# Optimization experiments

Hardware: AMD Instinct MI355X
Metric: run time of the kernel (lower is better)

Reference implementation:

```python
import jax, jax.numpy as jnp
import numpy as np

B, C, T, D = 4, 64, 256, 256   # batch, channel, time, in_feat
H, DK, OUT = 4, 64, 256        # heads, d_k, out_feat
MIN_VALUE = float(np.finfo(np.float32).min)


def _complex_linear(xr, xi, wr, wi, br, bi):
    # ComplexLinear: (fc_r(xr) - fc_i(xi), fc_r(xi) + fc_i(xr))
    out_r = (xr @ wr + br) - (xi @ wi + bi)
    out_i = (xi @ wr + br) + (xr @ wi + bi)
    return out_r, out_i


def setup_inputs() -> dict:
    key = jax.random.key(0)
    ks = jax.random.split(key, 23)
    s = 1.0 / np.sqrt(D)
    inp = {}
    names = ['q_r', 'q_i', 'k_r', 'k_i', 'v_r', 'v_i']
    for i, n in enumerate(names):
        inp[n] = jax.random.normal(ks[i], (B, C, T, D), dtype=jnp.float32)
    inp['mask'] = jnp.ones((B, 1, C), dtype=jnp.int32)
    pi = 6
    for proj in ['q', 'k', 'v', 'o']:
        out_dim = OUT if proj == 'o' else D
        inp[f'w{proj}_r'] = jax.random.normal(ks[pi], (D, out_dim), dtype=jnp.float32) * s; pi += 1
        inp[f'w{proj}_i'] = jax.random.normal(ks[pi], (D, out_dim), dtype=jnp.float32) * s; pi += 1
        inp[f'b{proj}_r'] = jax.random.normal(ks[pi], (out_dim,), dtype=jnp.float32) * 0.01; pi += 1
        inp[f'b{proj}_i'] = jax.random.normal(ks[pi], (out_dim,), dtype=jnp.float32) * 0.01; pi += 1
    return inp


def _split_heads(x):
    # (B, C, T, D) -> (B, H, T, C, DK)  [view + transpose(1,3)]
    return x.reshape(B, C, T, H, DK).transpose(0, 3, 2, 1, 4)


def _attention(q_r, q_i, k_r, k_i, v_r, v_i, mask,
               wq_r, wq_i, bq_r, bq_i, wk_r, wk_i, bk_r, bk_i,
               wv_r, wv_i, bv_r, bv_i, wo_r, wo_i, bo_r, bo_i):
    qr, qi = _complex_linear(q_r, q_i, wq_r, wq_i, bq_r, bq_i)
    kr, ki = _complex_linear(k_r, k_i, wk_r, wk_i, bk_r, bk_i)
    vr, vi = _complex_linear(v_r, v_i, wv_r, wv_i, bv_r, bv_i)
    qr, qi, kr, ki, vr, vi = map(_split_heads, (qr, qi, kr, ki, vr, vi))

    # scores = conj(q) @ k^T  (conjugate_transpose_matmul_conjugate), scaled by 1/sqrt(d_k)
    scale = 1.0 / np.sqrt(DK)
    s_r = (jnp.einsum('bhtcd,bhted->bhtce', qr, kr)
           + jnp.einsum('bhtcd,bhted->bhtce', qi, ki)) * scale
    s_i = (jnp.einsum('bhtcd,bhted->bhtce', qr, ki)
           - jnp.einsum('bhtcd,bhted->bhtce', qi, kr)) * scale

    # amplitude softmax with masking (mask: (B,1,C) -> (B,1,1,1,C), eq(0))
    mask_b = (mask == 0)[:, None, None]  # (B,1,1,1,C)
    amp = jnp.sqrt(s_r * s_r + s_i * s_i)
    amp = jnp.where(mask_b, MIN_VALUE, amp)
    sc = jax.nn.softmax(amp, axis=-1) / amp
    a_r = jnp.where(mask_b, 0.0, sc * s_r)
    a_i = jnp.where(mask_b, 0.0, sc * s_i)

    # complex matmul attn @ v
    x_r = (jnp.einsum('bhtce,bhted->bhtcd', a_r, vr)
           - jnp.einsum('bhtce,bhted->bhtcd', a_i, vi))
    x_i = (jnp.einsum('bhtce,bhted->bhtcd', a_i, vr)
           + jnp.einsum('bhtce,bhted->bhtcd', a_r, vi))

    # (B,H,T,C,DK) -> (B,C,T,H*DK)
    x_r = x_r.transpose(0, 3, 2, 1, 4).reshape(B, C, T, H * DK)
    x_i = x_i.transpose(0, 3, 2, 1, 4).reshape(B, C, T, H * DK)
    return _complex_linear(x_r, x_i, wo_r, wo_i, bo_r, bo_i)


def reference(q_r, q_i, k_r, k_i, v_r, v_i, mask,
              wq_r, wq_i, bq_r, bq_i, wk_r, wk_i, bk_r, bk_i,
              wv_r, wv_i, bv_r, bv_i, wo_r, wo_i, bo_r, bo_i):
    return _attention(q_r, q_i, k_r, k_i, v_r, v_i, mask,
                      wq_r, wq_i, bq_r, bq_i, wk_r, wk_i, bk_r, bk_i,
                      wv_r, wv_i, bv_r, bv_i, wo_r, wo_i, bo_r, bo_i)
```

## Files before the change

### kernel.cpp

```cpp
#include <hip/hip_runtime.h>
#include <hip/hip_bf16.h>
#include <cstddef>

#define MIN_VALUE_F (-3.402823466e38f)


typedef __attribute__((ext_vector_type(8))) __bf16 bfrag;
typedef __attribute__((ext_vector_type(4))) float f32x4;

__device__ __forceinline__ float bf2f(unsigned int u) {
    union { unsigned int i; float f; } v; v.i = u << 16; return v.f;
}
__device__ __forceinline__ unsigned short f2bf(float f) {
    union { float f; unsigned int i; } v; v.f = f;
    return (unsigned short)((v.i + 0x7fffu + ((v.i >> 16) & 1u)) >> 16);
}
__device__ __forceinline__ unsigned int cvt2(float a, float b) {
    __hip_bfloat16 lo = __float2bfloat16(a);
    __hip_bfloat16 hi = __float2bfloat16(b);
    union { __hip_bfloat16 h[2]; unsigned int u; } x;
    x.h[0] = lo; x.h[1] = hi;
    return x.u;
}
__device__ __forceinline__ bfrag negf(bfrag v) {
    union { bfrag b; unsigned int u[4]; } x; x.b = v;
    #pragma unroll
    for (int i = 0; i < 4; ++i) x.u[i] ^= 0x80008000u;
    return x.b;
}

typedef __attribute__((address_space(3))) void lds_void_t;
typedef const __attribute__((address_space(1))) void gmem_void_t;
__device__ __forceinline__ void glds16(const void* g, void* l) {
    __builtin_amdgcn_global_load_lds((gmem_void_t*)g, (lds_void_t*)l, 16, 0, 0);
}

__device__ __forceinline__ bfrag rdfrag(const unsigned short* arr, int row, int slot) {
    const int s = slot ^ (row & 7);
    return *(const bfrag*)&arr[row * 64 + s * 8];
}

__global__ __launch_bounds__(256)
void wprep_kernel(const float* __restrict__ w0, const float* __restrict__ w1,
                  const float* __restrict__ w2, const float* __restrict__ w3,
                  const float* __restrict__ w4, const float* __restrict__ w5,
                  unsigned short* __restrict__ dst)
{
    const int my = blockIdx.y;
    const float* wsrc[6] = {w0, w1, w2, w3, w4, w5};
    const float* w = wsrc[my];
    const int cid = blockIdx.x * 256 + threadIdx.x;
    const int img = cid >> 10;
    const int nb = img >> 2, s = img & 3;
    const int u0 = (cid & 1023) << 3;
    const int n_loc = u0 >> 6;
    const int k_src = (u0 & 63) ^ ((n_loc & 7) << 3);
    const int n = nb * 128 + n_loc;
    const int kbase = s * 64 + k_src;
    unsigned int p[4];
    #pragma unroll
    for (int jj = 0; jj < 4; ++jj) {
        const float a = w[(size_t)(kbase + 2 * jj) * 256 + n];
        const float b = w[(size_t)(kbase + 2 * jj + 1) * 256 + n];
        p[jj] = cvt2(a, b);
    }
    uint4 q; q.x = p[0]; q.y = p[1]; q.z = p[2]; q.w = p[3];
    *(uint4*)&dst[(size_t)my * 65536 + img * 8192 + u0] = q;
}

__global__ __launch_bounds__(512, 2)
void proj_mfma(const float* __restrict__ xq_r, const float* __restrict__ xq_i,
               const float* __restrict__ xk_r, const float* __restrict__ xk_i,
               const float* __restrict__ xv_r, const float* __restrict__ xv_i,
               const unsigned short* __restrict__ wimg,
               const float* __restrict__ bq_r, const float* __restrict__ bq_i,
               const float* __restrict__ bk_r, const float* __restrict__ bk_i,
               const float* __restrict__ bv_r, const float* __restrict__ bv_i,
               unsigned short* __restrict__ ws_out)
{
    __shared__ __align__(16) unsigned short SH[32768];
    unsigned short* As_r = SH;
    unsigned short* As_i = SH + 8192;
    unsigned short* Ws_r = SH + 16384;
    unsigned short* Ws_i = SH + 24576;

    const int pz = blockIdx.z;
    const float *xr, *xi, *br_, *bi_;
    if (pz == 0)      { xr = xq_r; xi = xq_i; br_ = bq_r; bi_ = bq_i; }
    else if (pz == 1) { xr = xk_r; xi = xk_i; br_ = bk_r; bi_ = bk_i; }
    else              { xr = xv_r; xi = xv_i; br_ = bv_r; bi_ = bv_i; }
    const unsigned short* wr_img = wimg + (size_t)pz * 131072;
    const unsigned short* wi_img = wr_img + 65536;
    unsigned short* outr = ws_out + (size_t)pz * 2 * 16777216;
    unsigned short* outi = outr + 16777216;

    const int tid = threadIdx.x;
    const int lane = tid & 63, wv = tid >> 6;
    const int l15 = lane & 15;
    const int wm = (wv >> 2) * 64, wn = (wv & 3) * 32;
    const int m0 = blockIdx.x * 128;
    const int nb = blockIdx.y;

    const int srow = tid >> 2;
    const int skq = (tid & 3) << 4;
    const int swz = (srow & 7) << 3;
    const int rowb = srow * 64;
    const float* arp = xr + (size_t)(m0 + srow) * 256 + skq;
    const float* aip = xi + (size_t)(m0 + srow) * 256 + skq;
    const uint4* wr32 = (const uint4*)(wr_img + nb * 4 * 8192);
    const uint4* wi32 = (const uint4*)(wi_img + nb * 4 * 8192);

    f32x4 accR[4][2] = {}, accI[4][2] = {};
    float4 ar4[4], ai4[4];
    uint4 wbr0, wbr1, wbi0, wbi1;

    auto load_step = [&](int s) {
        const float* a = arp + s * 64;
        const float* b = aip + s * 64;
        #pragma unroll
        for (int j = 0; j < 4; ++j) {
            ar4[j] = ((const float4*)a)[j];
            ai4[j] = ((const float4*)b)[j];
        }
        wbr0 = wr32[s * 1024 + tid];
        wbr1 = wr32[s * 1024 + 512 + tid];
        wbi0 = wi32[s * 1024 + tid];
        wbi1 = wi32[s * 1024 + 512 + tid];
    };
    auto write_stage = [&]() {
        uint4 p0, p1, q0, q1;
        p0.x = cvt2(ar4[0].x, ar4[0].y); p0.y = cvt2(ar4[0].z, ar4[0].w);
        p0.z = cvt2(ar4[1].x, ar4[1].y); p0.w = cvt2(ar4[1].z, ar4[1].w);
        p1.x = cvt2(ar4[2].x, ar4[2].y); p1.y = cvt2(ar4[2].z, ar4[2].w);
        p1.z = cvt2(ar4[3].x, ar4[3].y); p1.w = cvt2(ar4[3].z, ar4[3].w);
        q0.x = cvt2(ai4[0].x, ai4[0].y); q0.y = cvt2(ai4[0].z, ai4[0].w);
        q0.z = cvt2(ai4[1].x, ai4[1].y); q0.w = cvt2(ai4[1].z, ai4[1].w);
        q1.x = cvt2(ai4[2].x, ai4[2].y); q1.y = cvt2(ai4[2].z, ai4[2].w);
        q1.z = cvt2(ai4[3].x, ai4[3].y); q1.w = cvt2(ai4[3].z, ai4[3].w);
        *(uint4*)&As_r[rowb + (skq ^ swz)] = p0;
        *(uint4*)&As_r[rowb + ((skq + 8) ^ swz)] = p1;
        *(uint4*)&As_i[rowb + (skq ^ swz)] = q0;
        *(uint4*)&As_i[rowb + ((skq + 8) ^ swz)] = q1;
        *(uint4*)&Ws_r[tid * 8] = wbr0;
        *(uint4*)&Ws_r[4096 + tid * 8] = wbr1;
        *(uint4*)&Ws_i[tid * 8] = wbi0;
        *(uint4*)&Ws_i[4096 + tid * 8] = wbi1;
    };

    load_step(0);
    write_stage();
    __syncthreads();

    #pragma unroll
    for (int s = 0; s < 4; ++s) {
        if (s < 3) load_step(s + 1);
        #pragma unroll
        for (int ks = 0; ks < 2; ++ks) {
            const int kb = ks * 32 + ((lane >> 4) << 3);
            bfrag ar[4], ai[4], nai[4];
            #pragma unroll
            for (int mf = 0; mf < 4; ++mf) {
                const int m = wm + mf * 16 + l15;
                const int idx = m * 64 + (kb ^ ((m & 7) << 3));
                ar[mf] = *(const bfrag*)&As_r[idx];
                ai[mf] = *(const bfrag*)&As_i[idx];
                nai[mf] = negf(ai[mf]);
            }
            #pragma unroll
            for (int nf = 0; nf < 2; ++nf) {
                const int n = wn + nf * 16 + l15;
                const int idx = n * 64 + (kb ^ ((n & 7) << 3));
                const bfrag brf = *(const bfrag*)&Ws_r[idx];
                const bfrag bif = *(const bfrag*)&Ws_i[idx];
                #pragma unroll
                for (int mf = 0; mf < 4; ++mf) {
                    accR[mf][nf] = __builtin_amdgcn_mfma_f32_16x16x32_bf16(ar[mf], brf, accR[mf][nf], 0, 0, 0);
                    accR[mf][nf] = __builtin_amdgcn_mfma_f32_16x16x32_bf16(nai[mf], bif, accR[mf][nf], 0, 0, 0);
                    accI[mf][nf] = __builtin_amdgcn_mfma_f32_16x16x32_bf16(ai[mf], brf, accI[mf][nf], 0, 0, 0);
                    accI[mf][nf] = __builtin_amdgcn_mfma_f32_16x16x32_bf16(ar[mf], bif, accI[mf][nf], 0, 0, 0);
                }
            }
        }
        __syncthreads();
        if (s < 3) { write_stage(); __syncthreads(); }
    }

    const int bc = m0 >> 8, b = bc >> 6, c = bc & 63, t0 = m0 & 255;
    const int rowL = (lane >> 4) << 2;
    #pragma unroll
    for (int nf = 0; nf < 2; ++nf) {
        const int n_loc = wn + nf * 16 + l15;
        const int n_glob = nb * 128 + n_loc;
        const int hs = n_loc >> 6, dk = n_loc & 63;
        const float vbr = br_[n_glob], vbi = bi_[n_glob];
        const float addR = vbr - vbi, addI = vbr + vbi;
        #pragma unroll
        for (int mf = 0; mf < 4; ++mf) {
            const int tr = wm + mf * 16 + rowL;
            #pragma unroll
            for (int r = 0; r < 4; ++r) {
                const int L = hs * 8192 + (tr + r) * 64 + dk;
                SH[L] = f2bf(accR[mf][nf][r] + addR);
                SH[16384 + L] = f2bf(accI[mf][nf][r] + addI);
            }
        }
    }
    __syncthreads();
    const int h0 = nb * 2;
    #pragma unroll
    for (int p = 0; p < 4; ++p) {
        const int L = p * 4096 + tid * 8;
        const int hs2 = L >> 13, tr2 = (L >> 6) & 127, dk2 = L & 63;
        const size_t g = (((size_t)(b * 4 + h0 + hs2) * 256 + (t0 + tr2)) * 64 + c) * 64 + dk2;
        *(uint4*)&outr[g] = *(const uint4*)&SH[L];
        *(uint4*)&outi[g] = *(const uint4*)&SH[16384 + L];
    }
}

__global__ __launch_bounds__(256)
void attn_mfma(const unsigned short* __restrict__ Qg_r, const unsigned short* __restrict__ Qg_i,
               const unsigned short* __restrict__ Kg_r, const unsigned short* __restrict__ Kg_i,
               const unsigned short* __restrict__ Vg_r, const unsigned short* __restrict__ Vg_i,
               const int* __restrict__ mask,
               unsigned short* __restrict__ Xr, unsigned short* __restrict__ Xi)
{
    __shared__ __align__(16) unsigned short sQr[4096], sQi[4096];
    __shared__ __align__(16) unsigned short sKr[4096], sKi[4096];
    __shared__ __align__(16) unsigned short sVr[4608], sVi[4608];
    __shared__ int smask[64];

    const int bht = blockIdx.x;
    const int b = bht >> 10;
    const int h = (bht >> 8) & 3;
    const int t = bht & 255;
    const size_t base = (size_t)bht * 4096;
    const int tid = threadIdx.x;
    const int lane = tid & 63, wv = tid >> 6;
    const int l15 = lane & 15, hi = lane >> 4;

    const int ep = (lane & 31) * 2;
    const int dch = wv * 2 + (lane >> 5);
    const unsigned short* vr0p = Vg_r + base + (size_t)ep * 64 + dch * 8;
    const unsigned short* vi0p = Vg_i + base + (size_t)ep * 64 + dch * 8;
    const uint4 vr0 = *(const uint4*)vr0p;
    const uint4 vr1 = *(const uint4*)(vr0p + 64);
    const uint4 vi0 = *(const uint4*)vi0p;
    const uint4 vi1 = *(const uint4*)(vi0p + 64);

    #pragma unroll
    for (int i = 0; i < 2; ++i) {
        const int ch = wv * 128 + i * 64 + lane;
        const int r = ch >> 3, cg = ch & 7;
        const int so = r * 64 + ((cg ^ (r & 7)) << 3);
        const int dofs = (wv * 128 + i * 64) << 3;
        glds16(Qg_r + base + so, &sQr[dofs]);
        glds16(Qg_i + base + so, &sQi[dofs]);
        glds16(Kg_r + base + so, &sKr[dofs]);
        glds16(Kg_i + base + so, &sKi[dofs]);
    }
    if (tid < 64) smask[tid] = mask[b * 64 + tid];

    {
        union { uint4 v; unsigned short s[8]; } ar0, ar1, ai0, ai1;
        ar0.v = vr0; ar1.v = vr1; ai0.v = vi0; ai1.v = vi1;
        #pragma unroll
        for (int j = 0; j < 8; ++j) {
            const int d = dch * 8 + j;
            *(unsigned int*)&sVr[d * 72 + ep] = (unsigned)ar0.s[j] | ((unsigned)ar1.s[j] << 16);
            *(unsigned int*)&sVi[d * 72 + ep] = (unsigned)ai0.s[j] | ((unsigned)ai1.s[j] << 16);
        }
    }
    __syncthreads();

    const int cq = wv * 16 + l15;
    f32x4 aR[4] = {}, aI[4] = {};
    #pragma unroll
    for (int ks = 0; ks < 2; ++ks) {
        const int slot = ks * 4 + hi;
        const bfrag qr = rdfrag(sQr, cq, slot);
        const bfrag qi = rdfrag(sQi, cq, slot);
        const bfrag nqi = negf(qi);
        #pragma unroll
        for (int et = 0; et < 4; ++et) {
            const int re = et * 16 + l15;
            const bfrag kr = rdfrag(sKr, re, slot);
            const bfrag ki = rdfrag(sKi, re, slot);
            aR[et] = __builtin_amdgcn_mfma_f32_16x16x32_bf16(kr, qr, aR[et], 0, 0, 0);
            aR[et] = __builtin_amdgcn_mfma_f32_16x16x32_bf16(ki, qi, aR[et], 0, 0, 0);
            aI[et] = __builtin_amdgcn_mfma_f32_16x16x32_bf16(ki, qr, aI[et], 0, 0, 0);
            aI[et] = __builtin_amdgcn_mfma_f32_16x16x32_bf16(kr, nqi, aI[et], 0, 0, 0);
        }
    }
    __syncthreads();

    const float scale = 0.125f;
    float amp[4][4], ex[4][4];
    float mx = MIN_VALUE_F;
    #pragma unroll
    for (int et = 0; et < 4; ++et) {
        #pragma unroll
        for (int r = 0; r < 4; ++r) {
            const float sr = aR[et][r] * scale;
            const float si = aI[et][r] * scale;
            float a = sqrtf(fmaf(sr, sr, si * si));
            if (smask[et * 16 + hi * 4 + r] == 0) a = MIN_VALUE_F;
            amp[et][r] = a;
            mx = fmaxf(mx, a);
        }
    }
    mx = fmaxf(mx, __shfl_xor(mx, 16, 64));
    mx = fmaxf(mx, __shfl_xor(mx, 32, 64));
    float sm = 0.f;
    #pragma unroll
    for (int et = 0; et < 4; ++et) {
        #pragma unroll
        for (int r = 0; r < 4; ++r) {
            const float e_ = expf(amp[et][r] - mx);
            ex[et][r] = e_; sm += e_;
        }
    }
    sm += __shfl_xor(sm, 16, 64);
    sm += __shfl_xor(sm, 32, 64);

    #pragma unroll
    for (int et = 0; et < 4; ++et) {
        float pr[4], pi[4];
        #pragma unroll
        for (int r = 0; r < 4; ++r) {
            const float w = ex[et][r] * __builtin_amdgcn_rcpf(sm * amp[et][r]);
            pr[r] = w * (aR[et][r] * scale);
            pi[r] = w * (aI[et][r] * scale);
        }
        const int pidx = cq * 64 + ((et * 16 + hi * 4) ^ ((cq & 7) << 3));
        uint2 ur, ui;
        ur.x = cvt2(pr[0], pr[1]); ur.y = cvt2(pr[2], pr[3]);
        ui.x = cvt2(pi[0], pi[1]); ui.y = cvt2(pi[2], pi[3]);
        *(uint2*)&sQr[pidx] = ur;
        *(uint2*)&sQi[pidx] = ui;
    }
    __syncthreads();

    f32x4 xR4[4] = {}, xI4[4] = {};
    #pragma unroll
    for (int ks = 0; ks < 2; ++ks) {
        const int slot = ks * 4 + hi;
        const bfrag pr = rdfrag(sQr, cq, slot);
        const bfrag pi = rdfrag(sQi, cq, slot);
        const bfrag npi = negf(pi);
        #pragma unroll
        for (int dt = 0; dt < 4; ++dt) {
            const int rd = dt * 16 + l15;
            const bfrag vr = *(const bfrag*)&sVr[rd * 72 + ks * 32 + hi * 8];
            const bfrag vi = *(const bfrag*)&sVi[rd * 72 + ks * 32 + hi * 8];
            xR4[dt] = __builtin_amdgcn_mfma_f32_16x16x32_bf16(pr, vr, xR4[dt], 0, 0, 0);
            xR4[dt] = __builtin_amdgcn_mfma_f32_16x16x32_bf16(npi, vi, xR4[dt], 0, 0, 0);
            xI4[dt] = __builtin_amdgcn_mfma_f32_16x16x32_bf16(pi, vr, xI4[dt], 0, 0, 0);
            xI4[dt] = __builtin_amdgcn_mfma_f32_16x16x32_bf16(pr, vi, xI4[dt], 0, 0, 0);
        }
    }

    #pragma unroll
    for (int dt = 0; dt < 4; ++dt) {
        #pragma unroll
        for (int r = 0; r < 4; ++r) {
            const int c = wv * 16 + hi * 4 + r;
            const size_t o = (((size_t)(b * 64 + c) * 256) + t) * 256 + h * 64 + dt * 16 + l15;
            Xr[o] = f2bf(xR4[dt][r]);
            Xi[o] = f2bf(xI4[dt][r]);
        }
    }
}

__global__ __launch_bounds__(512, 2)
void oproj_mfma(const unsigned short* __restrict__ Xr_g, const unsigned short* __restrict__ Xi_g,
                const unsigned short* __restrict__ wimg,
                const float* __restrict__ bo_r, const float* __restrict__ bo_i,
                float* __restrict__ outr, float* __restrict__ outi)
{
    __shared__ __align__(16) unsigned short SH[32768];
    unsigned short* As_r = SH;
    unsigned short* As_i = SH + 8192;
    unsigned short* Ws_r = SH + 16384;
    unsigned short* Ws_i = SH + 24576;

    const int tid = threadIdx.x;
    const int lane = tid & 63, wv = tid >> 6;
    const int l15 = lane & 15;
    const int wm = (wv >> 2) * 64, wn = (wv & 3) * 32;
    const int m0 = blockIdx.x * 128;
    const int nb = blockIdx.y;

    const int srow = tid >> 2;
    const int skq = (tid & 3) << 4;
    const int swz = (srow & 7) << 3;
    const int rowb = srow * 64;
    const unsigned short* xrp = Xr_g + (size_t)(m0 + srow) * 256 + skq;
    const unsigned short* xip = Xi_g + (size_t)(m0 + srow) * 256 + skq;
    const uint4* wr32 = (const uint4*)(wimg + nb * 4 * 8192);
    const uint4* wi32 = (const uint4*)(wimg + 65536 + nb * 4 * 8192);

    f32x4 accR[4][2] = {}, accI[4][2] = {};
    uint4 xbr0, xbr1, xbi0, xbi1, wbr0, wbr1, wbi0, wbi1;

    auto load_step = [&](int s) {
        const uint4* a = (const uint4*)(xrp + s * 64);
        const uint4* bpt = (const uint4*)(xip + s * 64);
        xbr0 = a[0]; xbr1 = a[1];
        xbi0 = bpt[0]; xbi1 = bpt[1];
        wbr0 = wr32[s * 1024 + tid];
        wbr1 = wr32[s * 1024 + 512 + tid];
        wbi0 = wi32[s * 1024 + tid];
        wbi1 = wi32[s * 1024 + 512 + tid];
    };
    auto write_stage = [&]() {
        *(uint4*)&As_r[rowb + (skq ^ swz)] = xbr0;
        *(uint4*)&As_r[rowb + ((skq + 8) ^ swz)] = xbr1;
        *(uint4*)&As_i[rowb + (skq ^ swz)] = xbi0;
        *(uint4*)&As_i[rowb + ((skq + 8) ^ swz)] = xbi1;
        *(uint4*)&Ws_r[tid * 8] = wbr0;
        *(uint4*)&Ws_r[4096 + tid * 8] = wbr1;
        *(uint4*)&Ws_i[tid * 8] = wbi0;
        *(uint4*)&Ws_i[4096 + tid * 8] = wbi1;
    };

    load_step(0);
    write_stage();
    __syncthreads();

    #pragma unroll
    for (int s = 0; s < 4; ++s) {
        if (s < 3) load_step(s + 1);
        #pragma unroll
        for (int ks = 0; ks < 2; ++ks) {
            const int kb = ks * 32 + ((lane >> 4) << 3);
            bfrag ar[4], ai[4], nai[4];
            #pragma unroll
            for (int mf = 0; mf < 4; ++mf) {
                const int m = wm + mf * 16 + l15;
                const int idx = m * 64 + (kb ^ ((m & 7) << 3));
                ar[mf] = *(const bfrag*)&As_r[idx];
                ai[mf] = *(const bfrag*)&As_i[idx];
                nai[mf] = negf(ai[mf]);
            }
            #pragma unroll
            for (int nf = 0; nf < 2; ++nf) {
                const int n = wn + nf * 16 + l15;
                const int idx = n * 64 + (kb ^ ((n & 7) << 3));
                const bfrag brf = *(const bfrag*)&Ws_r[idx];
                const bfrag bif = *(const bfrag*)&Ws_i[idx];
                #pragma unroll
                for (int mf = 0; mf < 4; ++mf) {
                    accR[mf][nf] = __builtin_amdgcn_mfma_f32_16x16x32_bf16(ar[mf], brf, accR[mf][nf], 0, 0, 0);
                    accR[mf][nf] = __builtin_amdgcn_mfma_f32_16x16x32_bf16(nai[mf], bif, accR[mf][nf], 0, 0, 0);
                    accI[mf][nf] = __builtin_amdgcn_mfma_f32_16x16x32_bf16(ai[mf], brf, accI[mf][nf], 0, 0, 0);
                    accI[mf][nf] = __builtin_amdgcn_mfma_f32_16x16x32_bf16(ar[mf], bif, accI[mf][nf], 0, 0, 0);
                }
            }
        }
        __syncthreads();
        if (s < 3) { write_stage(); __syncthreads(); }
    }

    const int rowL = (lane >> 4) << 2;
    #pragma unroll
    for (int nf = 0; nf < 2; ++nf) {
        const int n = nb * 128 + wn + nf * 16 + l15;
        const float vbr = bo_r[n], vbi = bo_i[n];
        const float addR = vbr - vbi, addI = vbr + vbi;
        #pragma unroll
        for (int mf = 0; mf < 4; ++mf) {
            const int mb = m0 + wm + mf * 16 + rowL;
            #pragma unroll
            for (int r = 0; r < 4; ++r) {
                const size_t o = (size_t)(mb + r) * 256 + n;
                outr[o] = accR[mf][nf][r] + addR;
                outi[o] = accI[mf][nf][r] + addI;
            }
        }
    }
}

extern "C" void kernel_launch(void* const* d_in, const int* in_sizes, int n_in,
                              void* d_out, int out_size, void* d_ws, size_t ws_size,
                              hipStream_t stream)
{
    (void)in_sizes; (void)n_in; (void)out_size; (void)ws_size;
    const float* q_r = (const float*)d_in[0];
    const float* q_i = (const float*)d_in[1];
    const float* k_r = (const float*)d_in[2];
    const float* k_i = (const float*)d_in[3];
    const float* v_r = (const float*)d_in[4];
    const float* v_i = (const float*)d_in[5];
    const int* mask = (const int*)d_in[6];
    const float* wq_r = (const float*)d_in[7];
    const float* wq_i = (const float*)d_in[8];
    const float* bq_r = (const float*)d_in[9];
    const float* bq_i = (const float*)d_in[10];
    const float* wk_r = (const float*)d_in[11];
    const float* wk_i = (const float*)d_in[12];
    const float* bk_r = (const float*)d_in[13];
    const float* bk_i = (const float*)d_in[14];
    const float* wv_r = (const float*)d_in[15];
    const float* wv_i = (const float*)d_in[16];
    const float* bv_r = (const float*)d_in[17];
    const float* bv_i = (const float*)d_in[18];
    const float* wo_r = (const float*)d_in[19];
    const float* wo_i = (const float*)d_in[20];
    const float* bo_r = (const float*)d_in[21];
    const float* bo_i = (const float*)d_in[22];

    const size_t TS = 16777216;
    unsigned short* ws = (unsigned short*)d_ws;
    unsigned short* Q = ws;
    unsigned short* Xr = ws + 6 * TS;
    unsigned short* Xi = ws + 7 * TS;
    unsigned short* wimg_qkv = ws + 6 * TS;
    unsigned short* wimg_o = ws;

    wprep_kernel<<<dim3(32, 6), 256, 0, stream>>>(wq_r, wq_i, wk_r, wk_i, wv_r, wv_i, wimg_qkv);
    proj_mfma<<<dim3(512, 2, 3), 512, 0, stream>>>(q_r, q_i, k_r, k_i, v_r, v_i, wimg_qkv,
                                                   bq_r, bq_i, bk_r, bk_i, bv_r, bv_i, ws);
    attn_mfma<<<dim3(4096), 256, 0, stream>>>(Q, Q + TS, Q + 2 * TS, Q + 3 * TS,
                                              Q + 4 * TS, Q + 5 * TS, mask, Xr, Xi);
    wprep_kernel<<<dim3(32, 2), 256, 0, stream>>>(wo_r, wo_i, wo_r, wo_r, wo_r, wo_r, wimg_o);
    oproj_mfma<<<dim3(512, 2), 512, 0, stream>>>(Xr, Xi, wimg_o, bo_r, bo_i,
                                                 (float*)d_out, (float*)d_out + TS);
}
```

Before: 350.5 us.

## Double-buffer projection GEMMs with K=32 stages and direct global-to-LDS loads

Restructures the input and output projection GEMMs to use two LDS buffers of K=32 slices across 8 stages instead of a single K=64 buffer across 4 stages. Weight tiles, and in oproj the bf16 activations too, are now copied with global_load_lds directly into the next buffer while the current one is consumed, and the weight image layout and swizzle are rewritten to match. This removes one barrier per stage and the register staging. Launch bounds are raised to 4 blocks per CU to increase occupancy, which constrains register use. Shared memory per block stays at 64 KB.

```diff
diff --git a/kernel.cpp b/kernel.cpp
--- a/kernel.cpp
+++ b/kernel.cpp
@@ -50,25 +50,24 @@
     const float* wsrc[6] = {w0, w1, w2, w3, w4, w5};
     const float* w = wsrc[my];
     const int cid = blockIdx.x * 256 + threadIdx.x;
-    const int img = cid >> 10;
-    const int nb = img >> 2, s = img & 3;
-    const int u0 = (cid & 1023) << 3;
-    const int n_loc = u0 >> 6;
-    const int k_src = (u0 & 63) ^ ((n_loc & 7) << 3);
-    const int n = nb * 128 + n_loc;
-    const int kbase = s * 64 + k_src;
+    const int ss = cid & 3;
+    const int n  = (cid >> 2) & 127;
+    const int s  = (cid >> 9) & 7;
+    const int nb = (cid >> 12) & 1;
+    const int nn = nb * 128 + n;
+    const int kb = s * 32 + ((ss ^ ((n >> 1) & 3)) << 3);
     unsigned int p[4];
     #pragma unroll
     for (int jj = 0; jj < 4; ++jj) {
-        const float a = w[(size_t)(kbase + 2 * jj) * 256 + n];
-        const float b = w[(size_t)(kbase + 2 * jj + 1) * 256 + n];
+        const float a = w[(size_t)(kb + 2 * jj) * 256 + nn];
+        const float b = w[(size_t)(kb + 2 * jj + 1) * 256 + nn];
         p[jj] = cvt2(a, b);
     }
     uint4 q; q.x = p[0]; q.y = p[1]; q.z = p[2]; q.w = p[3];
-    *(uint4*)&dst[(size_t)my * 65536 + img * 8192 + u0] = q;
-}
-
-__global__ __launch_bounds__(512, 2)
+    *(uint4*)&dst[(size_t)my * 65536 + (size_t)cid * 8] = q;
+}
+
+__global__ __launch_bounds__(512, 4)
 void proj_mfma(const float* __restrict__ xq_r, const float* __restrict__ xq_i,
                const float* __restrict__ xk_r, const float* __restrict__ xk_i,
                const float* __restrict__ xv_r, const float* __restrict__ xv_i,
@@ -79,110 +78,95 @@
                unsigned short* __restrict__ ws_out)
 {
     __shared__ __align__(16) unsigned short SH[32768];
-    unsigned short* As_r = SH;
-    unsigned short* As_i = SH + 8192;
-    unsigned short* Ws_r = SH + 16384;
-    unsigned short* Ws_i = SH + 24576;
 
     const int pz = blockIdx.z;
     const float *xr, *xi, *br_, *bi_;
     if (pz == 0)      { xr = xq_r; xi = xq_i; br_ = bq_r; bi_ = bq_i; }
     else if (pz == 1) { xr = xk_r; xi = xk_i; br_ = bk_r; bi_ = bk_i; }
     else              { xr = xv_r; xi = xv_i; br_ = bv_r; bi_ = bv_i; }
-    const unsigned short* wr_img = wimg + (size_t)pz * 131072;
-    const unsigned short* wi_img = wr_img + 65536;
     unsigned short* outr = ws_out + (size_t)pz * 2 * 16777216;
     unsigned short* outi = outr + 16777216;
 
     const int tid = threadIdx.x;
     const int lane = tid & 63, wv = tid >> 6;
-    const int l15 = lane & 15;
+    const int l15 = lane & 15, hi = lane >> 4;
     const int wm = (wv >> 2) * 64, wn = (wv & 3) * 32;
     const int m0 = blockIdx.x * 128;
     const int nb = blockIdx.y;
 
-    const int srow = tid >> 2;
-    const int skq = (tid & 3) << 4;
-    const int swz = (srow & 7) << 3;
-    const int rowb = srow * 64;
-    const float* arp = xr + (size_t)(m0 + srow) * 256 + skq;
-    const float* aip = xi + (size_t)(m0 + srow) * 256 + skq;
-    const uint4* wr32 = (const uint4*)(wr_img + nb * 4 * 8192);
-    const uint4* wi32 = (const uint4*)(wi_img + nb * 4 * 8192);
+    const unsigned short* wr_img = wimg + (size_t)pz * 131072 + nb * 32768;
+    const unsigned short* wi_img = wr_img + 65536;
+
+    const int arow = tid >> 3;
+    const int apos = tid & 7;
+    float4 fr0, fr1, fi0, fi1;
 
     f32x4 accR[4][2] = {}, accI[4][2] = {};
-    float4 ar4[4], ai4[4];
-    uint4 wbr0, wbr1, wbi0, wbi1;
-
-    auto load_step = [&](int s) {
-        const float* a = arp + s * 64;
-        const float* b = aip + s * 64;
-        #pragma unroll
-        for (int j = 0; j < 4; ++j) {
-            ar4[j] = ((const float4*)a)[j];
-            ai4[j] = ((const float4*)b)[j];
-        }
-        wbr0 = wr32[s * 1024 + tid];
-        wbr1 = wr32[s * 1024 + 512 + tid];
-        wbi0 = wi32[s * 1024 + tid];
-        wbi1 = wi32[s * 1024 + 512 + tid];
+
+    auto loadA = [&](int s) {
+        const size_t o0 = (size_t)(m0 + arow) * 256 + s * 32 + apos * 4;
+        const size_t o1 = (size_t)(m0 + 64 + arow) * 256 + s * 32 + apos * 4;
+        fr0 = *(const float4*)(xr + o0);
+        fr1 = *(const float4*)(xr + o1);
+        fi0 = *(const float4*)(xi + o0);
+        fi1 = *(const float4*)(xi + o1);
     };
-    auto write_stage = [&]() {
-        uint4 p0, p1, q0, q1;
-        p0.x = cvt2(ar4[0].x, ar4[0].y); p0.y = cvt2(ar4[0].z, ar4[0].w);
-        p0.z = cvt2(ar4[1].x, ar4[1].y); p0.w = cvt2(ar4[1].z, ar4[1].w);
-        p1.x = cvt2(ar4[2].x, ar4[2].y); p1.y = cvt2(ar4[2].z, ar4[2].w);
-        p1.z = cvt2(ar4[3].x, ar4[3].y); p1.w = cvt2(ar4[3].z, ar4[3].w);
-        q0.x = cvt2(ai4[0].x, ai4[0].y); q0.y = cvt2(ai4[0].z, ai4[0].w);
-        q0.z = cvt2(ai4[1].x, ai4[1].y); q0.w = cvt2(ai4[1].z, ai4[1].w);
-        q1.x = cvt2(ai4[2].x, ai4[2].y); q1.y = cvt2(ai4[2].z, ai4[2].w);
-        q1.z = cvt2(ai4[3].x, ai4[3].y); q1.w = cvt2(ai4[3].z, ai4[3].w);
-        *(uint4*)&As_r[rowb + (skq ^ swz)] = p0;
-        *(uint4*)&As_r[rowb + ((skq + 8) ^ swz)] = p1;
-        *(uint4*)&As_i[rowb + (skq ^ swz)] = q0;
-        *(uint4*)&As_i[rowb + ((skq + 8) ^ swz)] = q1;
-        *(uint4*)&Ws_r[tid * 8] = wbr0;
-        *(uint4*)&Ws_r[4096 + tid * 8] = wbr1;
-        *(uint4*)&Ws_i[tid * 8] = wbi0;
-        *(uint4*)&Ws_i[4096 + tid * 8] = wbi1;
+    auto loadW = [&](int s, int buf) {
+        glds16(wr_img + s * 4096 + tid * 8, &SH[buf * 16384 + 8192 + tid * 8]);
+        glds16(wi_img + s * 4096 + tid * 8, &SH[buf * 16384 + 12288 + tid * 8]);
     };
-
-    load_step(0);
-    write_stage();
-    __syncthreads();
-
-    #pragma unroll
-    for (int s = 0; s < 4; ++s) {
-        if (s < 3) load_step(s + 1);
-        #pragma unroll
-        for (int ks = 0; ks < 2; ++ks) {
-            const int kb = ks * 32 + ((lane >> 4) << 3);
-            bfrag ar[4], ai[4], nai[4];
+    auto writeA = [&](int buf) {
+        const int r0 = arow, r1 = 64 + arow;
+        const int sw = (apos >> 1) ^ ((r0 >> 1) & 3);
+        const int hf = (apos & 1) * 4;
+        const int i0 = buf * 16384 + r0 * 32 + (sw << 3) + hf;
+        const int i1 = buf * 16384 + r1 * 32 + (sw << 3) + hf;
+        uint2 a;
+        a.x = cvt2(fr0.x, fr0.y); a.y = cvt2(fr0.z, fr0.w);
+        *(uint2*)&SH[i0] = a;
+        a.x = cvt2(fr1.x, fr1.y); a.y = cvt2(fr1.z, fr1.w);
+        *(uint2*)&SH[i1] = a;
+        a.x = cvt2(fi0.x, fi0.y); a.y = cvt2(fi0.z, fi0.w);
+        *(uint2*)&SH[4096 + i0] = a;
+        a.x = cvt2(fi1.x, fi1.y); a.y = cvt2(fi1.z, fi1.w);
+        *(uint2*)&SH[4096 + i1] = a;
+    };
+
+    loadA(0); loadW(0, 0); writeA(0);
+    __syncthreads();
+
+    for (int s = 0; s < 8; ++s) {
+        const int b = s & 1;
+        if (s < 7) { loadA(s + 1); loadW(s + 1, b ^ 1); }
+        const unsigned short* Ar = &SH[b * 16384];
+        const unsigned short* Ai = Ar + 4096;
+        const unsigned short* Wr = Ar + 8192;
+        const unsigned short* Wi = Ar + 12288;
+        bfrag ar[4], ai[4], nai[4];
+        #pragma unroll
+        for (int mf = 0; mf < 4; ++mf) {
+            const int m = wm + mf * 16 + l15;
+            const int idx = m * 32 + ((hi ^ ((m >> 1) & 3)) << 3);
+            ar[mf] = *(const bfrag*)&Ar[idx];
+            ai[mf] = *(const bfrag*)&Ai[idx];
+            nai[mf] = negf(ai[mf]);
+        }
+        #pragma unroll
+        for (int nf = 0; nf < 2; ++nf) {
+            const int n = wn + nf * 16 + l15;
+            const int idx = n * 32 + ((hi ^ ((n >> 1) & 3)) << 3);
+            const bfrag brf = *(const bfrag*)&Wr[idx];
+            const bfrag bif = *(const bfrag*)&Wi[idx];
             #pragma unroll
             for (int mf = 0; mf < 4; ++mf) {
-                const int m = wm + mf * 16 + l15;
-                const int idx = m * 64 + (kb ^ ((m & 7) << 3));
-                ar[mf] = *(const bfrag*)&As_r[idx];
-                ai[mf] = *(const bfrag*)&As_i[idx];
-                nai[mf] = negf(ai[mf]);
+                accR[mf][nf] = __builtin_amdgcn_mfma_f32_16x16x32_bf16(ar[mf], brf, accR[mf][nf], 0, 0, 0);
+                accR[mf][nf] = __builtin_amdgcn_mfma_f32_16x16x32_bf16(nai[mf], bif, accR[mf][nf], 0, 0, 0);
+                accI[mf][nf] = __builtin_amdgcn_mfma_f32_16x16x32_bf16(ai[mf], brf, accI[mf][nf], 0, 0, 0);
+                accI[mf][nf] = __builtin_amdgcn_mfma_f32_16x16x32_bf16(ar[mf], bif, accI[mf][nf], 0, 0, 0);
             }
-            #pragma unroll
-            for (int nf = 0; nf < 2; ++nf) {
-                const int n = wn + nf * 16 + l15;
-                const int idx = n * 64 + (kb ^ ((n & 7) << 3));
-                const bfrag brf = *(const bfrag*)&Ws_r[idx];
-                const bfrag bif = *(const bfrag*)&Ws_i[idx];
-                #pragma unroll
-                for (int mf = 0; mf < 4; ++mf) {
-                    accR[mf][nf] = __builtin_amdgcn_mfma_f32_16x16x32_bf16(ar[mf], brf, accR[mf][nf], 0, 0, 0);
-                    accR[mf][nf] = __builtin_amdgcn_mfma_f32_16x16x32_bf16(nai[mf], bif, accR[mf][nf], 0, 0, 0);
-                    accI[mf][nf] = __builtin_amdgcn_mfma_f32_16x16x32_bf16(ai[mf], brf, accI[mf][nf], 0, 0, 0);
-                    accI[mf][nf] = __builtin_amdgcn_mfma_f32_16x16x32_bf16(ar[mf], bif, accI[mf][nf], 0, 0, 0);
-                }
-            }
-        }
+        }
+        if (s < 7) writeA(b ^ 1);
         __syncthreads();
-        if (s < 3) { write_stage(); __syncthreads(); }
     }
 
     const int bc = m0 >> 8, b = bc >> 6, c = bc & 63, t0 = m0 & 255;
@@ -371,94 +355,74 @@
     }
 }
 
-__global__ __launch_bounds__(512, 2)
+__global__ __launch_bounds__(512, 4)
 void oproj_mfma(const unsigned short* __restrict__ Xr_g, const unsigned short* __restrict__ Xi_g,
                 const unsigned short* __restrict__ wimg,
                 const float* __restrict__ bo_r, const float* __restrict__ bo_i,
                 float* __restrict__ outr, float* __restrict__ outi)
 {
     __shared__ __align__(16) unsigned short SH[32768];
-    unsigned short* As_r = SH;
-    unsigned short* As_i = SH + 8192;
-    unsigned short* Ws_r = SH + 16384;
-    unsigned short* Ws_i = SH + 24576;
 
     const int tid = threadIdx.x;
     const int lane = tid & 63, wv = tid >> 6;
-    const int l15 = lane & 15;
+    const int l15 = lane & 15, hi = lane >> 4;
     const int wm = (wv >> 2) * 64, wn = (wv & 3) * 32;
     const int m0 = blockIdx.x * 128;
     const int nb = blockIdx.y;
 
-    const int srow = tid >> 2;
-    const int skq = (tid & 3) << 4;
-    const int swz = (srow & 7) << 3;
-    const int rowb = srow * 64;
-    const unsigned short* xrp = Xr_g + (size_t)(m0 + srow) * 256 + skq;
-    const unsigned short* xip = Xi_g + (size_t)(m0 + srow) * 256 + skq;
-    const uint4* wr32 = (const uint4*)(wimg + nb * 4 * 8192);
-    const uint4* wi32 = (const uint4*)(wimg + 65536 + nb * 4 * 8192);
+    const unsigned short* wr_img = wimg + nb * 32768;
+    const unsigned short* wi_img = wr_img + 65536;
+
+    const int xrow = tid >> 2;
+    const int xss  = tid & 3;
+    const int xslot = xss ^ ((xrow >> 1) & 3);
 
     f32x4 accR[4][2] = {}, accI[4][2] = {};
-    uint4 xbr0, xbr1, xbi0, xbi1, wbr0, wbr1, wbi0, wbi1;
-
-    auto load_step = [&](int s) {
-        const uint4* a = (const uint4*)(xrp + s * 64);
-        const uint4* bpt = (const uint4*)(xip + s * 64);
-        xbr0 = a[0]; xbr1 = a[1];
-        xbi0 = bpt[0]; xbi1 = bpt[1];
-        wbr0 = wr32[s * 1024 + tid];
-        wbr1 = wr32[s * 1024 + 512 + tid];
-        wbi0 = wi32[s * 1024 + tid];
-        wbi1 = wi32[s * 1024 + 512 + tid];
+
+    auto loadX = [&](int s, int buf) {
+        const size_t so = (size_t)(m0 + xrow) * 256 + s * 32 + xslot * 8;
+        glds16(Xr_g + so, &SH[buf * 16384 + tid * 8]);
+        glds16(Xi_g + so, &SH[buf * 16384 + 4096 + tid * 8]);
     };
-    auto write_stage = [&]() {
-        *(uint4*)&As_r[rowb + (skq ^ swz)] = xbr0;
-        *(uint4*)&As_r[rowb + ((skq + 8) ^ swz)] = xbr1;
-        *(uint4*)&As_i[rowb + (skq ^ swz)] = xbi0;
-        *(uint4*)&As_i[rowb + ((skq + 8) ^ swz)] = xbi1;
-        *(uint4*)&Ws_r[tid * 8] = wbr0;
-        *(uint4*)&Ws_r[4096 + tid * 8] = wbr1;
-        *(uint4*)&Ws_i[tid * 8] = wbi0;
-        *(uint4*)&Ws_i[4096 + tid * 8] = wbi1;
+    auto loadW = [&](int s, int buf) {
+        glds16(wr_img + s * 4096 + tid * 8, &SH[buf * 16384 + 8192 + tid * 8]);
+        glds16(wi_img + s * 4096 + tid * 8, &SH[buf * 16384 + 12288 + tid * 8]);
     };
 
-    load_step(0);
-    write_stage();
-    __syncthreads();
-
-    #pragma unroll
-    for (int s = 0; s < 4; ++s) {
-        if (s < 3) load_step(s + 1);
-        #pragma unroll
-        for (int ks = 0; ks < 2; ++ks) {
-            const int kb = ks * 32 + ((lane >> 4) << 3);
-            bfrag ar[4], ai[4], nai[4];
+    loadX(0, 0); loadW(0, 0);
+    __syncthreads();
+
+    for (int s = 0; s < 8; ++s) {
+        const int b = s & 1;
+        if (s < 7) { loadX(s + 1, b ^ 1); loadW(s + 1, b ^ 1); }
+        const unsigned short* Ar = &SH[b * 16384];
+        const unsigned short* Ai = Ar + 4096;
+        const unsigned short* Wr = Ar + 8192;
+        const unsigned short* Wi = Ar + 12288;
+        bfrag ar[4], ai[4], nai[4];
+        #pragma unroll
+        for (int mf = 0; mf < 4; ++mf) {
+            const int m = wm + mf * 16 + l15;
+            const int idx = m * 32 + ((hi ^ ((m >> 1) & 3)) << 3);
+            ar[mf] = *(const bfrag*)&Ar[idx];
+            ai[mf] = *(const bfrag*)&Ai[idx];
+            nai[mf] = negf(ai[mf]);
+        }
+        #pragma unroll
+        for (int nf = 0; nf < 2; ++nf) {
+            const int n = wn + nf * 16 + l15;
+            const int idx = n * 32 + ((hi ^ ((n >> 1) & 3)) << 3);
+            const bfrag brf = *(const bfrag*)&Wr[idx];
+            const bfrag bif = *(const bfrag*)&Wi[idx];
             #pragma unroll
             for (int mf = 0; mf < 4; ++mf) {
-                const int m = wm + mf * 16 + l15;
-                const int idx = m * 64 + (kb ^ ((m & 7) << 3));
-                ar[mf] = *(const bfrag*)&As_r[idx];
-                ai[mf] = *(const bfrag*)&As_i[idx];
-                nai[mf] = negf(ai[mf]);
+                accR[mf][nf] = __builtin_amdgcn_mfma_f32_16x16x32_bf16(ar[mf], brf, accR[mf][nf], 0, 0, 0);
+                accR[mf][nf] = __builtin_amdgcn_mfma_f32_16x16x32_bf16(nai[mf], bif, accR[mf][nf], 0, 0, 0);
+                accI[mf][nf] = __builtin_amdgcn_mfma_f32_16x16x32_bf16(ai[mf], brf, accI[mf][nf], 0, 0, 0);
+                accI[mf][nf] = __builtin_amdgcn_mfma_f32_16x16x32_bf16(ar[mf], bif, accI[mf][nf], 0, 0, 0);
             }
-            #pragma unroll
-            for (int nf = 0; nf < 2; ++nf) {
-                const int n = wn + nf * 16 + l15;
-                const int idx = n * 64 + (kb ^ ((n & 7) << 3));
-                const bfrag brf = *(const bfrag*)&Ws_r[idx];
-                const bfrag bif = *(const bfrag*)&Ws_i[idx];
-                #pragma unroll
-                for (int mf = 0; mf < 4; ++mf) {
-                    accR[mf][nf] = __builtin_amdgcn_mfma_f32_16x16x32_bf16(ar[mf], brf, accR[mf][nf], 0, 0, 0);
-                    accR[mf][nf] = __builtin_amdgcn_mfma_f32_16x16x32_bf16(nai[mf], bif, accR[mf][nf], 0, 0, 0);
-                    accI[mf][nf] = __builtin_amdgcn_mfma_f32_16x16x32_bf16(ai[mf], brf, accI[mf][nf], 0, 0, 0);
-                    accI[mf][nf] = __builtin_amdgcn_mfma_f32_16x16x32_bf16(ar[mf], bif, accI[mf][nf], 0, 0, 0);
-                }
-            }
         }
         __syncthreads();
-        if (s < 3) { write_stage(); __syncthreads(); }
     }
 
     const int rowL = (lane >> 4) << 2;
```

Result: slower. 562.3 us (+60.4%).
